# Performance work log

Measured on AMD Instinct MI355X. Metric: run time of the kernel, lower is better.

The kernel has to match this reference:

```python
import jax, jax.numpy as jnp
import numpy as np

B, N, C_SA, OUT = 16, 2048, 512, 1024
BN_EPS = 1e-5


def pconv(x, w, b=None):
    # 1x1 Conv1d: x [B,Cin,N], w [Cout,Cin] -> [B,Cout,N]
    y = jnp.einsum('oc,bcn->bon', w, x)
    return y if b is None else y + b[None, :, None]


def setup_inputs() -> dict:
    key = jax.random.key(0)
    ks = jax.random.split(key, 16)
    s = lambda k, shape: jax.random.normal(k, shape, dtype=jnp.float32) * 0.05
    return {
        'x': jax.random.normal(ks[0], (B, 3, N), dtype=jnp.float32),
        'w1': s(ks[1], (128, 21)), 'b1': s(ks[2], (128,)),
        'w2': s(ks[3], (256, 128)), 'b2': s(ks[4], (256,)),
        'w3': s(ks[5], (512, 512)), 'b3': s(ks[6], (512,)),
        'w4': s(ks[7], (OUT, 512)), 'b4': s(ks[8], (OUT,)),
        'wqk': s(ks[9], (C_SA // 4, C_SA)),            # q_conv.weight tied to k_conv.weight, no bias
        'wv': s(ks[10], (C_SA, C_SA)), 'bv': s(ks[11], (C_SA,)),
        'wt': s(ks[12], (C_SA, C_SA)), 'bt': s(ks[13], (C_SA,)),
        'gamma': jnp.ones((C_SA,), dtype=jnp.float32),
        'beta': jnp.zeros((C_SA,), dtype=jnp.float32),
    }


def reference(x, w1, b1, w2, b2, w3, b3, w4, b4, wqk, wv, bv, wt, bt, gamma, beta):
    b, _, n = x.shape
    # positional encoding on [B,N,3]: [t, sin(t*2^i), cos(t*2^i)] for i in 0..2 -> 21 channels
    t = jnp.transpose(x, (0, 2, 1))
    enc = [t]
    for f in (1.0, 2.0, 4.0):
        enc.append(jnp.sin(t * f))
        enc.append(jnp.cos(t * f))
    h = jnp.transpose(jnp.concatenate(enc, axis=-1), (0, 2, 1))  # [B,21,N]

    h = jax.nn.relu(pconv(h, w1, b1))               # [B,128,N]
    h = pconv(h, w2, b2)                            # [B,256,N]
    g = jnp.max(h, axis=2)                          # [B,256]
    h = jnp.concatenate([h, jnp.broadcast_to(g[:, :, None], (b, g.shape[1], n))], axis=1)  # [B,512,N]
    h = jax.nn.relu(pconv(h, w3, b3))               # [B,512,N]

    # SA_Layer (offset attention, double normalization)
    xq = jnp.einsum('oc,bcn->bno', wqk, h)          # [B,N,128]
    xk = jnp.einsum('oc,bcn->bon', wqk, h)          # [B,128,N]
    xv = pconv(h, wv, bv)                           # [B,512,N]
    energy = jnp.einsum('bqo,bok->bqk', xq, xk)     # [B,N,N]
    attn = jax.nn.softmax(energy, axis=-1)
    attn = attn / (1e-9 + jnp.sum(attn, axis=1, keepdims=True))  # L1 renorm over query dim
    x_r = jnp.einsum('bck,bqk->bcq', xv, attn)      # x_v @ attn^T -> [B,512,N]
    d = pconv(h - x_r, wt, bt)
    # BatchNorm1d, training mode (batch statistics, biased variance)
    mu = jnp.mean(d, axis=(0, 2))
    var = jnp.var(d, axis=(0, 2))
    d = gamma[None, :, None] * (d - mu[None, :, None]) * jax.lax.rsqrt(var + BN_EPS)[None, :, None] + beta[None, :, None]
    h = h + jax.nn.relu(d)

    h = pconv(h, w4, b4)                            # [B,OUT,N]
    return jnp.max(h, axis=2)                       # [B,OUT]
```

## Files before the change

kernel.cpp:

```cpp
#include <hip/hip_runtime.h>
#include <cmath>

#define GN 2048
#define GB 16

typedef __attribute__((ext_vector_type(8))) short bf8_t;
typedef __attribute__((ext_vector_type(4))) float f4_t;

__device__ __forceinline__ short f2bf(float f) {
    union { float f; unsigned u; } v; v.f = f;
    unsigned r = v.u + 0x7FFFu + ((v.u >> 16) & 1u);
    return (short)(r >> 16);
}
__device__ __forceinline__ float bf2f(short s) {
    union { unsigned u; float f; } v; v.u = ((unsigned)(unsigned short)s) << 16;
    return v.f;
}

__device__ __forceinline__ void load16_lds(const short* g, short* l) {
    __builtin_amdgcn_global_load_lds(
        (const __attribute__((address_space(1))) unsigned int*)g,
        (__attribute__((address_space(3))) unsigned int*)l, 16, 0, 0);
}

__device__ __forceinline__ float wave_max(float v) {
#pragma unroll
    for (int o = 32; o > 0; o >>= 1) v = fmaxf(v, __shfl_xor(v, o, 64));
    return v;
}
__device__ __forceinline__ float wave_sum(float v) {
#pragma unroll
    for (int o = 32; o > 0; o >>= 1) v += __shfl_xor(v, o, 64);
    return v;
}
__device__ __forceinline__ float block_sum(float v) {
    __shared__ float sm[4];
    v = wave_sum(v);
    if ((threadIdx.x & 63) == 0) sm[threadIdx.x >> 6] = v;
    __syncthreads();
    v = sm[0] + sm[1] + sm[2] + sm[3];
    __syncthreads();
    return v;
}

__global__ __launch_bounds__(256) void f2ball_k(
    const float* __restrict__ w2, const float* __restrict__ w3,
    const float* __restrict__ wqk, const float* __restrict__ wv,
    const float* __restrict__ wt, const float* __restrict__ w4,
    short* __restrict__ dst) {
    int i = blockIdx.x * 256 + threadIdx.x;
    if (i >= 1409024) return;
    float v;
    if (i < 32768) v = w2[i];
    else if (i < 294912) v = w3[i - 32768];
    else if (i < 360448) v = wqk[i - 294912];
    else if (i < 622592) v = wv[i - 360448];
    else if (i < 884736) v = wt[i - 622592];
    else v = w4[i - 884736];
    dst[i] = f2bf(v);
}

__global__ __launch_bounds__(256) void posenc_conv1_k(
    const float* __restrict__ x, const float* __restrict__ w1,
    const float* __restrict__ b1, short* __restrict__ h1) {
    __shared__ float w[128 * 21];
    __shared__ float bb[128];
    __shared__ float se[256][21];
    const int tid = threadIdx.x;
    for (int i = tid; i < 128 * 21; i += 256) w[i] = w1[i];
    if (tid < 128) bb[tid] = b1[tid];
    int p0 = blockIdx.x * 256;
    int p = p0 + tid, b = p >> 11, n = p & (GN - 1);
    const float* xb = x + (long)b * 3 * GN + n;
    float t0 = xb[0], t1 = xb[GN], t2 = xb[2 * GN];
    se[tid][0] = t0; se[tid][1] = t1; se[tid][2] = t2;
    se[tid][3] = sinf(t0); se[tid][4] = sinf(t1); se[tid][5] = sinf(t2);
    se[tid][6] = cosf(t0); se[tid][7] = cosf(t1); se[tid][8] = cosf(t2);
    se[tid][9] = sinf(2.f * t0); se[tid][10] = sinf(2.f * t1); se[tid][11] = sinf(2.f * t2);
    se[tid][12] = cosf(2.f * t0); se[tid][13] = cosf(2.f * t1); se[tid][14] = cosf(2.f * t2);
    se[tid][15] = sinf(4.f * t0); se[tid][16] = sinf(4.f * t1); se[tid][17] = sinf(4.f * t2);
    se[tid][18] = cosf(4.f * t0); se[tid][19] = cosf(4.f * t1); se[tid][20] = cosf(4.f * t2);
    __syncthreads();
    short* outb = h1 + (long)p0 * 128;
    for (int it = 0; it < 128; ++it) {
        int L = it * 256 + tid;
        int pl = L >> 7, o = L & 127;
        float s = bb[o];
        const float* er = se[pl];
        const float* wr = &w[o * 21];
#pragma unroll
        for (int c = 0; c < 21; ++c) s = fmaf(wr[c], er[c], s);
        outb[L] = f2bf(fmaxf(s, 0.f));
    }
}

template <int MODE, int BIAS, bool RELU, bool STATS = false, bool COLMAX = false>
__global__ __launch_bounds__(256) void mm_k(
    const short* __restrict__ A, int lda, long long aB,
    const short* __restrict__ B, int ldb, long long bB,
    const float* __restrict__ bias, int biasStride,
    const short* __restrict__ aux, long long auxB,
    const float* __restrict__ rsv,
    float* __restrict__ Cf, long long cfB,
    short* __restrict__ Cb, long long cbB,
    float* __restrict__ Pmax, float* __restrict__ Ps2,
    int ldc, int K) {
    const int z = blockIdx.z;
    A += (long long)z * aB;
    B += (long long)z * bB;
    if (MODE == 4) { aux += (long long)z * auxB; rsv += (long long)z * GN; }
    if (MODE == 1) Cf += (long long)z * cfB;
    if (MODE == 2 || MODE == 4 || MODE == 6) Cb += (long long)z * cbB;
    if (MODE == 6) Pmax += (long long)z * GN * 32;
    const int row0 = blockIdx.x * 128, col0 = blockIdx.y * 128;
    const int tid = threadIdx.x;
    const int lane = tid & 63, w = tid >> 6;
    const int r = lane & 15, q = lane >> 4;
    const int wr = w >> 1, wc = w & 1;

    __shared__ short lA[8192];
    __shared__ short lB[8192];

    f4_t acc[4][4] = {};

    const int sRow = lane >> 2;
    const int sKb = (lane & 3) ^ ((lane >> 3) & 3);
    const long aG = (long)(row0 + w * 32 + sRow) * lda + sKb * 8;
    const long bG = (long)(col0 + w * 32 + sRow) * ldb + sKb * 8;
    short* ldsA0 = lA + (w * 32) * 32;
    short* ldsA1 = lA + (w * 32 + 16) * 32;
    short* ldsB0 = lB + (w * 32) * 32;
    short* ldsB1 = lB + (w * 32 + 16) * 32;

    const int sw = (q ^ ((r >> 1) & 3)) * 8;
    int aoff[4], boff[4];
#pragma unroll
    for (int i = 0; i < 4; ++i) {
        aoff[i] = (wr * 64 + i * 16 + r) * 32 + sw;
        boff[i] = (wc * 64 + i * 16 + r) * 32 + sw;
    }

    for (int k0 = 0; k0 < K; k0 += 64) {
        __syncthreads();
        load16_lds(A + aG + k0, ldsA0);
        load16_lds(A + aG + (long)16 * lda + k0, ldsA1);
        load16_lds(B + bG + k0, ldsB0);
        load16_lds(B + bG + (long)16 * ldb + k0, ldsB1);
        load16_lds(A + aG + k0 + 32, ldsA0 + 4096);
        load16_lds(A + aG + (long)16 * lda + k0 + 32, ldsA1 + 4096);
        load16_lds(B + bG + k0 + 32, ldsB0 + 4096);
        load16_lds(B + bG + (long)16 * ldb + k0 + 32, ldsB1 + 4096);
        asm volatile("s_waitcnt vmcnt(0)" ::: "memory");
        __syncthreads();
#pragma unroll
        for (int h = 0; h < 2; ++h) {
            const short* la = lA + h * 4096;
            const short* lb = lB + h * 4096;
            bf8_t av[4], bv[4];
#pragma unroll
            for (int i = 0; i < 4; ++i) av[i] = *(const bf8_t*)(la + aoff[i]);
#pragma unroll
            for (int j = 0; j < 4; ++j) bv[j] = *(const bf8_t*)(lb + boff[j]);
#pragma unroll
            for (int i = 0; i < 4; ++i)
#pragma unroll
                for (int j = 0; j < 4; ++j)
                    acc[i][j] = __builtin_amdgcn_mfma_f32_16x16x32_bf16(av[i], bv[j], acc[i][j], 0, 0, 0);
        }
    }

    if constexpr (MODE == 5) {
        int b = row0 >> 11;
        int rw = (blockIdx.x * 2 + wr) & 31;
#pragma unroll
        for (int j = 0; j < 4; ++j) {
            float vm = -1e30f;
#pragma unroll
            for (int i = 0; i < 4; ++i)
#pragma unroll
                for (int e = 0; e < 4; ++e) vm = fmaxf(vm, acc[i][j][e]);
            vm = fmaxf(vm, __shfl_xor(vm, 16, 64));
            vm = fmaxf(vm, __shfl_xor(vm, 32, 64));
            if (q == 0) {
                int gcol = col0 + wc * 64 + j * 16 + r;
                Pmax[(((long)b * 1024 + gcol) << 5) + rw] = vm + bias[gcol];
            }
        }
    } else if constexpr (MODE == 6) {
        float rsum[4][4] = {};
#pragma unroll
        for (int j = 0; j < 4; ++j) {
            int gcol = col0 + wc * 64 + j * 16 + r;
#pragma unroll
            for (int i = 0; i < 4; ++i) {
#pragma unroll
                for (int e = 0; e < 4; ++e) {
                    int grow = row0 + wr * 64 + i * 16 + q * 4 + e;
                    float ex = __expf(acc[i][j][e]);
                    rsum[i][e] += ex;
                    Cb[(long)grow * ldc + gcol] = f2bf(ex);
                }
            }
        }
#pragma unroll
        for (int i = 0; i < 4; ++i)
#pragma unroll
            for (int e = 0; e < 4; ++e) {
                float v = rsum[i][e];
                v += __shfl_xor(v, 1, 64);
                v += __shfl_xor(v, 2, 64);
                v += __shfl_xor(v, 4, 64);
                v += __shfl_xor(v, 8, 64);
                if (r == 0) {
                    int grow = row0 + wr * 64 + i * 16 + q * 4 + e;
                    Pmax[((long)grow << 5) + blockIdx.y * 2 + wc] = v;
                }
            }
    } else if constexpr (MODE == 4) {
#pragma unroll
        for (int i = 0; i < 4; ++i) {
#pragma unroll
            for (int e = 0; e < 4; ++e) {
                int grow = row0 + wr * 64 + i * 16 + q * 4 + e;
                float rsr = rsv[grow];
                long ob = (long)grow * ldc + col0 + wc * 64 + r;
#pragma unroll
                for (int j = 0; j < 4; ++j) {
                    long off = ob + j * 16;
                    Cb[off] = f2bf(bf2f(aux[off]) - acc[i][j][e] * rsr);
                }
            }
        }
    } else {
        const int b2d = (BIAS == 3) ? (row0 >> 11) : 0;
#pragma unroll
        for (int j = 0; j < 4; ++j) {
            int gcol = col0 + wc * 64 + j * 16 + r;
            float bvv = 0.f;
            if constexpr (BIAS == 1) bvv = bias[gcol];
            if constexpr (BIAS == 3) bvv = bias[b2d * biasStride + gcol];
            float s1 = 0.f, s2 = 0.f;
            float cmx = -1e30f;
#pragma unroll
            for (int i = 0; i < 4; ++i) {
#pragma unroll
                for (int e = 0; e < 4; ++e) {
                    int grow = row0 + wr * 64 + i * 16 + q * 4 + e;
                    float v = acc[i][j][e] + bvv;
                    if constexpr (BIAS == 2) v += bias[grow];
                    if constexpr (RELU) v = fmaxf(v, 0.f);
                    if constexpr (STATS) { s1 += v; s2 = fmaf(v, v, s2); }
                    if constexpr (COLMAX) cmx = fmaxf(cmx, v);
                    long off = (long)grow * ldc + gcol;
                    if constexpr (MODE == 1) Cf[off] = v;
                    if constexpr (MODE == 2) Cb[off] = f2bf(v);
                }
            }
            if constexpr (STATS) {
                s1 += __shfl_xor(s1, 16, 64); s1 += __shfl_xor(s1, 32, 64);
                s2 += __shfl_xor(s2, 16, 64); s2 += __shfl_xor(s2, 32, 64);
                if (q == 0) {
                    int rw2 = blockIdx.x * 2 + wr;
                    Pmax[rw2 * 512 + gcol] = s1;
                    Ps2[rw2 * 512 + gcol] = s2;
                }
            }
            if constexpr (COLMAX) {
                cmx = fmaxf(cmx, __shfl_xor(cmx, 16, 64));
                cmx = fmaxf(cmx, __shfl_xor(cmx, 32, 64));
                if (q == 0) {
                    int b = row0 >> 11;
                    int rw = (blockIdx.x * 2 + wr) & 31;
                    Pmax[(((long)b * ldc + gcol) << 5) + rw] = cmx;
                }
            }
        }
    }
}

__global__ __launch_bounds__(256) void rs_k(const float* __restrict__ rp,
                                            float* __restrict__ rs) {
    int i = blockIdx.x * 256 + threadIdx.x;
    const float* p = rp + ((long)i << 5);
    float s = 0.f;
#pragma unroll
    for (int j = 0; j < 32; ++j) s += p[j];
    rs[i] = 1.f / s;
}

__global__ __launch_bounds__(256) void maxg_k(const float* __restrict__ P,
                                              float* __restrict__ g) {
    int i = blockIdx.x * 256 + threadIdx.x;
    const float* p = P + ((long)i << 5);
    float m = p[0];
#pragma unroll
    for (int j = 1; j < 32; ++j) m = fmaxf(m, p[j]);
    g[i] = m;
}

__global__ __launch_bounds__(256) void cvec_k(const float* __restrict__ w3,
                                              const float* __restrict__ b3,
                                              const float* __restrict__ g,
                                              float* __restrict__ cvec) {
    int idx = blockIdx.x * 256 + threadIdx.x;
    int b = idx >> 9, o = idx & 511;
    const float* gb = g + (b << 8);
    const float* wr = w3 + (long)o * 512 + 256;
    float s = b3[o];
    for (int c = 0; c < 256; ++c) s = fmaf(wr[c], gb[c], s);
    cvec[idx] = s;
}

__global__ __launch_bounds__(256) void colsum1_k(const short* __restrict__ Ab,
                                                 const float* __restrict__ rs,
                                                 float* __restrict__ cp) {
    int kb = blockIdx.x, qs = blockIdx.y, z = blockIdx.z;
    int k = kb * 256 + threadIdx.x;
    const short* p = Ab + (long)z * GN * GN + (long)qs * 64 * GN + k;
    const float* rv = rs + z * GN + qs * 64;
    float s = 0.f;
    for (int qq = 0; qq < 64; ++qq) s += bf2f(p[(long)qq * GN]) * rv[qq];
    cp[((z * 32 + qs) * GN) + k] = s;
}
__global__ __launch_bounds__(256) void colsum2_k(const float* __restrict__ cp,
                                                 float* __restrict__ cs) {
    int k = blockIdx.x * 256 + threadIdx.x, z = blockIdx.y;
    float s = 1e-9f;
    for (int qs = 0; qs < 32; ++qs) s += cp[((z * 32 + qs) * GN) + k];
    cs[z * GN + k] = s;
}

__global__ __launch_bounds__(256) void xvscale_k(short* __restrict__ xvc,
                                                 const float* __restrict__ cs) {
    long idx = ((long)blockIdx.x * 256 + threadIdx.x) * 4;
    int p = (int)(idx & 32767);
    short* ptr = xvc + idx;
    float4 cv = *(const float4*)(cs + p);
    uint2 u = *(const uint2*)ptr;
    short* sp = (short*)&u;
    sp[0] = f2bf(bf2f(sp[0]) / cv.x);
    sp[1] = f2bf(bf2f(sp[1]) / cv.y);
    sp[2] = f2bf(bf2f(sp[2]) / cv.z);
    sp[3] = f2bf(bf2f(sp[3]) / cv.w);
    *(uint2*)ptr = u;
}

__global__ __launch_bounds__(256) void bn2_k(const float* __restrict__ bs1,
                                             const float* __restrict__ bs2,
                                             const float* __restrict__ gamma,
                                             const float* __restrict__ beta,
                                             float* __restrict__ sc,
                                             float* __restrict__ sh) {
    int c = blockIdx.x;
    float s = 0.f, s2 = 0.f;
    for (int i = threadIdx.x; i < 512; i += 256) {
        s += bs1[i * 512 + c];
        s2 += bs2[i * 512 + c];
    }
    s = block_sum(s);
    s2 = block_sum(s2);
    if (threadIdx.x == 0) {
        const float cnt = (float)(GB * GN);
        float mu = s / cnt;
        float var = s2 / cnt - mu * mu;
        float r = rsqrtf(var + 1e-5f);
        float gm = gamma[c] * r;
        sc[c] = gm;
        sh[c] = beta[c] - gm * mu;
    }
}

__global__ __launch_bounds__(256) void bn_apply_k(const short* __restrict__ h3b,
                                                  const short* __restrict__ d,
                                                  const float* __restrict__ sc,
                                                  const float* __restrict__ sh,
                                                  short* __restrict__ h4) {
    long bidx = ((long)blockIdx.x * 256 + threadIdx.x) * 4;
    int c = (int)(bidx & 511);
    uint2 du = *(const uint2*)(d + bidx);
    short* ds = (short*)&du;
    uint2 hu = *(const uint2*)(h3b + bidx);
    short* hs = (short*)&hu;
    float4 a4 = *(const float4*)(sc + c);
    float4 b4 = *(const float4*)(sh + c);
    float r0 = bf2f(hs[0]) + fmaxf(fmaf(bf2f(ds[0]), a4.x, b4.x), 0.f);
    float r1 = bf2f(hs[1]) + fmaxf(fmaf(bf2f(ds[1]), a4.y, b4.y), 0.f);
    float r2 = bf2f(hs[2]) + fmaxf(fmaf(bf2f(ds[2]), a4.z, b4.z), 0.f);
    float r3 = bf2f(hs[3]) + fmaxf(fmaf(bf2f(ds[3]), a4.w, b4.w), 0.f);
    uint2 o;
    o.x = (unsigned short)f2bf(r0) | ((unsigned)(unsigned short)f2bf(r1) << 16);
    o.y = (unsigned short)f2bf(r2) | ((unsigned)(unsigned short)f2bf(r3) << 16);
    *(uint2*)(h4 + bidx) = o;
}

__global__ __launch_bounds__(256) void max_final_k(const float* __restrict__ P,
                                                   float* __restrict__ out) {
    int i = blockIdx.x * 256 + threadIdx.x;
    const float* p = P + ((long)i << 5);
    float m = p[0];
#pragma unroll
    for (int j = 1; j < 32; ++j) m = fmaxf(m, p[j]);
    out[i] = m;
}

extern "C" void kernel_launch(void* const* d_in, const int* in_sizes, int n_in,
                              void* d_out, int out_size, void* d_ws, size_t ws_size,
                              hipStream_t stream) {
    const float* x = (const float*)d_in[0];
    const float* w1 = (const float*)d_in[1];
    const float* b1 = (const float*)d_in[2];
    const float* w2 = (const float*)d_in[3];
    const float* b2 = (const float*)d_in[4];
    const float* w3 = (const float*)d_in[5];
    const float* b3 = (const float*)d_in[6];
    const float* w4 = (const float*)d_in[7];
    const float* b4 = (const float*)d_in[8];
    const float* wqk = (const float*)d_in[9];
    const float* wv = (const float*)d_in[10];
    const float* bv = (const float*)d_in[11];
    const float* wt = (const float*)d_in[12];
    const float* bt = (const float*)d_in[13];
    const float* gamma = (const float*)d_in[14];
    const float* beta = (const float*)d_in[15];
    float* out = (float*)d_out;

    char* base = (char*)d_ws;
    short* h3b = (short*)base;
    short* hsT = (short*)(base + 33554432);
    short* kT  = (short*)(base + 67108864);
    short* xvc = (short*)(base + 75497472);
    short* EA  = (short*)(base + 109051904);
    short* h1T = (short*)(base + 109051904);
    short* h2T = (short*)(base + 117440512);
    short* dTb = (short*)(base + 109051904);
    short* h4T = (short*)(base + 67108864);
    char* S = base + 243269632;
    float* g    = (float*)(S + 262144);
    float* cvec = (float*)(S + 278528);
    float* cp   = (float*)(S + 311296);
    float* rp   = cp;
    float* cs   = (float*)(S + 4505600);
    float* bs1  = (float*)(S + 4636672);
    float* bs2  = (float*)(S + 5685248);
    float* bnsc = (float*)(S + 6733824);
    float* bnsh = (float*)(S + 6735872);
    float* Pmax = (float*)(S + 6737920);
    short* w2b  = (short*)(S + 8835072);
    short* w3b  = (short*)(S + 8900608);
    short* wqkb = (short*)(S + 9424896);
    short* wvb  = (short*)(S + 9555968);
    short* wtb  = (short*)(S + 10080256);
    short* w4b  = (short*)(S + 10604544);
    float* rs   = (float*)(S + 11653120);

    f2ball_k<<<5505, 256, 0, stream>>>(w2, w3, wqk, wv, wt, w4, w2b);

    posenc_conv1_k<<<128, 256, 0, stream>>>(x, w1, b1, h1T);

    mm_k<2, 1, false, false, true><<<dim3(256, 2, 1), 256, 0, stream>>>(
        h1T, 128, 0, w2b, 128, 0, b2, 0, nullptr, 0, nullptr,
        nullptr, 0, h2T, 0, Pmax, nullptr, 256, 128);

    maxg_k<<<16, 256, 0, stream>>>(Pmax, g);

    cvec_k<<<32, 256, 0, stream>>>(w3, b3, g, cvec);

    mm_k<2, 3, true><<<dim3(256, 4, 1), 256, 0, stream>>>(
        h2T, 256, 0, w3b, 512, 0, cvec, 512, nullptr, 0, nullptr,
        nullptr, 0, h3b, 0, nullptr, nullptr, 512, 256);

    mm_k<2, 0, false><<<dim3(256, 1, 1), 256, 0, stream>>>(
        h3b, 512, 0, wqkb, 512, 0, nullptr, 0, nullptr, 0, nullptr,
        nullptr, 0, kT, 0, nullptr, nullptr, 128, 512);

    mm_k<2, 2, false><<<dim3(4, 256, 1), 256, 0, stream>>>(
        wvb, 512, 0, h3b, 512, 0, bv, 0, nullptr, 0, nullptr,
        nullptr, 0, xvc, 0, nullptr, nullptr, 32768, 512);

    mm_k<6, 0, false><<<dim3(16, 16, 16), 256, 0, stream>>>(
        kT, 128, (long long)GN * 128, kT, 128, (long long)GN * 128,
        nullptr, 0, nullptr, 0, nullptr, nullptr, 0,
        EA, (long long)GN * GN, rp, nullptr, GN, 128);
    rs_k<<<128, 256, 0, stream>>>(rp, rs);
    colsum1_k<<<dim3(8, 32, GB), 256, 0, stream>>>(EA, rs, cp);
    colsum2_k<<<dim3(8, GB), 256, 0, stream>>>(cp, cs);
    xvscale_k<<<16384, 256, 0, stream>>>(xvc, cs);
    mm_k<4, 0, false><<<dim3(16, 4, 16), 256, 0, stream>>>(
        EA, GN, (long long)GN * GN,
        xvc, 32768, (long long)GN,
        nullptr, 0,
        h3b, (long long)GN * 512, rs,
        nullptr, 0,
        hsT, (long long)GN * 512,
        nullptr, nullptr, 512, GN);

    mm_k<2, 1, false, true><<<dim3(256, 4, 1), 256, 0, stream>>>(
        hsT, 512, 0, wtb, 512, 0, bt, 0, nullptr, 0, nullptr,
        nullptr, 0, dTb, 0, bs1, bs2, 512, 512);

    bn2_k<<<512, 256, 0, stream>>>(bs1, bs2, gamma, beta, bnsc, bnsh);

    bn_apply_k<<<16384, 256, 0, stream>>>(h3b, dTb, bnsc, bnsh, h4T);

    mm_k<5, 1, false><<<dim3(256, 8, 1), 256, 0, stream>>>(
        h4T, 512, 0, w4b, 512, 0, b4, 0, nullptr, 0, nullptr,
        nullptr, 0, nullptr, 0, Pmax, nullptr, 1024, 512);

    max_final_k<<<64, 256, 0, stream>>>(Pmax, out);
}
```

Measured before the change: 500.2 us.

## Add 256x256-tile 8-wave GEMM kernel for attention-apply, wt and w4 matmuls

Adds a new GEMM kernel with a 256x256 output tile, 512 threads and double-buffered LDS staging. The global-to-LDS loads are interleaved with four MFMA quadrants per K-step, using barriers, priority raising and explicit waitcnt. It replaces the older kernel for the attention-times-V matmul, the wt projection with BN statistics, and the w4 projection with max pooling, to raise data reuse per tile and overlap loads with compute. The cost is heavier register and LDS use (128 KB of LDS per block) and fewer blocks per grid.

```diff
diff --git a/kernel.cpp b/kernel.cpp
--- a/kernel.cpp
+++ b/kernel.cpp
@@ -278,6 +278,213 @@
     }
 }
 
+__device__ __forceinline__ void stage2(const short* g0, const short* g1, short* dst) {
+    load16_lds(g0, dst);
+    load16_lds(g1, dst + 4096);
+}
+
+template <int MH, int NH>
+__device__ __forceinline__ void mfma_quad(const bf8_t (&av)[4][2], const bf8_t (&bv)[2][2],
+                                          f4_t (&acc)[8][4]) {
+#pragma unroll
+    for (int mi = 0; mi < 4; ++mi)
+#pragma unroll
+        for (int ni = 0; ni < 2; ++ni) {
+            acc[MH * 4 + mi][NH * 2 + ni] = __builtin_amdgcn_mfma_f32_16x16x32_bf16(
+                av[mi][0], bv[ni][0], acc[MH * 4 + mi][NH * 2 + ni], 0, 0, 0);
+            acc[MH * 4 + mi][NH * 2 + ni] = __builtin_amdgcn_mfma_f32_16x16x32_bf16(
+                av[mi][1], bv[ni][1], acc[MH * 4 + mi][NH * 2 + ni], 0, 0, 0);
+        }
+}
+
+__device__ __forceinline__ void rd4(const short* p, int swz0, int swz1, bf8_t (&v)[4][2]) {
+#pragma unroll
+    for (int i = 0; i < 4; ++i) {
+        v[i][0] = *(const bf8_t*)(p + i * 1024 + swz0);
+        v[i][1] = *(const bf8_t*)(p + i * 1024 + swz1);
+    }
+}
+__device__ __forceinline__ void rd2(const short* p, int swz0, int swz1, bf8_t (&v)[2][2]) {
+#pragma unroll
+    for (int i = 0; i < 2; ++i) {
+        v[i][0] = *(const bf8_t*)(p + i * 1024 + swz0);
+        v[i][1] = *(const bf8_t*)(p + i * 1024 + swz1);
+    }
+}
+
+#define SB0 __builtin_amdgcn_sched_barrier(0)
+#define BARRIER asm volatile("s_barrier" ::: "memory")
+
+template <int MODE, int BIAS, bool RELU, bool STATS = false>
+__global__ __launch_bounds__(512, 2) void mm256_k(
+    const short* __restrict__ A, int lda, long long aB,
+    const short* __restrict__ B, int ldb, long long bB,
+    const float* __restrict__ bias,
+    const short* __restrict__ aux, long long auxB,
+    const float* __restrict__ rsv,
+    short* __restrict__ Cb, long long cbB,
+    float* __restrict__ Pmax, float* __restrict__ Ps2,
+    int ldc, int K) {
+    __shared__ short lA[32768];
+    __shared__ short lB[32768];
+    const int z = blockIdx.z;
+    A += (long long)z * aB;
+    B += (long long)z * bB;
+    if constexpr (MODE == 4) { aux += (long long)z * auxB; rsv += (long long)z * GN; }
+    if constexpr (MODE != 5) Cb += (long long)z * cbB;
+    const int row0 = blockIdx.x * 256, col0 = blockIdx.y * 256;
+    const int tid = threadIdx.x;
+    const int lane = tid & 63, w = tid >> 6;
+    const int r16 = lane & 15, q = lane >> 4;
+    const int wr = w >> 2, wc = w & 3;
+
+    const int rc0 = w * 8 + (lane >> 3);
+    const int s8 = ((lane & 7) ^ (rc0 & 7)) * 8;
+    const long ldA64 = (long)64 * lda, ldB64 = (long)64 * ldb;
+    const short* aH0 = A + (long)(row0 + rc0) * lda + s8;
+    const short* aH1 = aH0 + (long)128 * lda;
+    const short* bH0 = B + (long)(col0 + rc0) * ldb + s8;
+    const short* bH1 = bH0 + (long)128 * ldb;
+    short* dA = lA + w * 512;
+    short* dB = lB + w * 512;
+
+#define STG_A(d_, h_, kt_) stage2((h_ ? aH1 : aH0) + (long)(kt_) * 64,                      \
+                                  (h_ ? aH1 : aH0) + (long)(kt_) * 64 + ldA64,              \
+                                  dA + (d_) * 16384 + (h_) * 8192)
+#define STG_B(d_, h_, kt_) stage2((h_ ? bH1 : bH0) + (long)(kt_) * 64,                      \
+                                  (h_ ? bH1 : bH0) + (long)(kt_) * 64 + ldB64,              \
+                                  dB + (d_) * 16384 + (h_) * 8192)
+
+    const int swz0 = (q ^ (r16 & 7)) * 8;
+    const int swz1 = ((4 + q) ^ (r16 & 7)) * 8;
+    const int arow = (wr * 64 + r16) * 64;
+    const int brow = (wc * 32 + r16) * 64;
+
+    f4_t acc[8][4] = {};
+    bf8_t av[4][2], bv0[2][2], bv1[2][2];
+    const int NT = K >> 6;
+
+    STG_A(0, 0, 0); STG_B(0, 0, 0); STG_B(0, 1, 0); STG_A(0, 1, 0);
+    STG_A(1, 0, 1); STG_B(1, 0, 1);
+    asm volatile("s_waitcnt vmcnt(4)" ::: "memory");
+    SB0; BARRIER; SB0;
+
+    for (int t = 0; t < NT; ++t) {
+        const int d = t & 1;
+        const short* la = lA + d * 16384;
+        const short* lb = lB + d * 16384;
+        rd4(la + arow, swz0, swz1, av);
+        rd2(lb + brow, swz0, swz1, bv0);
+        if (t + 1 < NT) STG_B(d ^ 1, 1, t + 1);
+        SB0; BARRIER; SB0;
+        __builtin_amdgcn_s_setprio(1);
+        mfma_quad<0, 0>(av, bv0, acc);
+        __builtin_amdgcn_s_setprio(0);
+        SB0; BARRIER; SB0;
+        rd2(lb + 8192 + brow, swz0, swz1, bv1);
+        if (t + 1 < NT) STG_A(d ^ 1, 1, t + 1);
+        SB0; BARRIER; SB0;
+        __builtin_amdgcn_s_setprio(1);
+        mfma_quad<0, 1>(av, bv1, acc);
+        __builtin_amdgcn_s_setprio(0);
+        SB0; BARRIER; SB0;
+        rd4(la + 8192 + arow, swz0, swz1, av);
+        if (t + 2 < NT) STG_A(d, 0, t + 2);
+        SB0; BARRIER; SB0;
+        __builtin_amdgcn_s_setprio(1);
+        mfma_quad<1, 0>(av, bv0, acc);
+        __builtin_amdgcn_s_setprio(0);
+        SB0; BARRIER; SB0;
+        if (t + 2 < NT) {
+            STG_B(d, 0, t + 2);
+            asm volatile("s_waitcnt vmcnt(4)" ::: "memory");
+        } else if (t + 1 < NT) {
+            asm volatile("s_waitcnt vmcnt(0)" ::: "memory");
+        }
+        SB0; BARRIER; SB0;
+        __builtin_amdgcn_s_setprio(1);
+        mfma_quad<1, 1>(av, bv1, acc);
+        __builtin_amdgcn_s_setprio(0);
+        SB0; BARRIER; SB0;
+    }
+#undef STG_A
+#undef STG_B
+
+    const int mrow = row0 + wr * 64 + q * 4;
+    const int ncol = col0 + wc * 32 + r16;
+
+    if constexpr (MODE == 4) {
+#pragma unroll
+        for (int m = 0; m < 8; ++m) {
+#pragma unroll
+            for (int e = 0; e < 4; ++e) {
+                const int grow = mrow + (m >> 2) * 128 + (m & 3) * 16 + e;
+                const float rsr = rsv[grow];
+                const long rb = (long)grow * ldc;
+#pragma unroll
+                for (int n = 0; n < 4; ++n) {
+                    const long off = rb + ncol + (n >> 1) * 128 + (n & 1) * 16;
+                    Cb[off] = f2bf(bf2f(aux[off]) - acc[m][n][e] * rsr);
+                }
+            }
+        }
+    } else if constexpr (MODE == 2) {
+#pragma unroll
+        for (int n = 0; n < 4; ++n) {
+            const int gcol = ncol + (n >> 1) * 128 + (n & 1) * 16;
+            float bvv = 0.f;
+            if constexpr (BIAS == 1) bvv = bias[gcol];
+#pragma unroll
+            for (int mh = 0; mh < 2; ++mh) {
+                float s1 = 0.f, s2 = 0.f;
+#pragma unroll
+                for (int mi = 0; mi < 4; ++mi) {
+#pragma unroll
+                    for (int e = 0; e < 4; ++e) {
+                        const int grow = mrow + mh * 128 + mi * 16 + e;
+                        float v = acc[mh * 4 + mi][n][e] + bvv;
+                        if constexpr (RELU) v = fmaxf(v, 0.f);
+                        if constexpr (STATS) { s1 += v; s2 = fmaf(v, v, s2); }
+                        Cb[(long)grow * ldc + gcol] = f2bf(v);
+                    }
+                }
+                if constexpr (STATS) {
+                    s1 += __shfl_xor(s1, 16, 64); s1 += __shfl_xor(s1, 32, 64);
+                    s2 += __shfl_xor(s2, 16, 64); s2 += __shfl_xor(s2, 32, 64);
+                    if (q == 0) {
+                        const int rw2 = blockIdx.x * 4 + mh * 2 + wr;
+                        Pmax[rw2 * 512 + gcol] = s1;
+                        Ps2[rw2 * 512 + gcol] = s2;
+                    }
+                }
+            }
+        }
+    } else if constexpr (MODE == 5) {
+        const int b = row0 >> 11;
+#pragma unroll
+        for (int n = 0; n < 4; ++n) {
+            const int gcol = ncol + (n >> 1) * 128 + (n & 1) * 16;
+            const float bvv = bias[gcol];
+#pragma unroll
+            for (int mh = 0; mh < 2; ++mh) {
+                float vm = -1e30f;
+#pragma unroll
+                for (int mi = 0; mi < 4; ++mi)
+#pragma unroll
+                    for (int e = 0; e < 4; ++e) vm = fmaxf(vm, acc[mh * 4 + mi][n][e]);
+                vm = fmaxf(vm, __shfl_xor(vm, 16, 64));
+                vm = fmaxf(vm, __shfl_xor(vm, 32, 64));
+                if (q == 0) {
+                    const int rw = (blockIdx.x * 4 + mh * 2 + wr) & 31;
+                    Pmax[(((long)b * ldc + gcol) << 5) + rw] = vm + bvv;
+                }
+            }
+        }
+    }
+}
+#undef SB0
+#undef BARRIER
+
 __global__ __launch_bounds__(256) void rs_k(const float* __restrict__ rp,
                                             float* __restrict__ rs) {
     int i = blockIdx.x * 256 + threadIdx.x;
@@ -485,26 +692,23 @@
     colsum1_k<<<dim3(8, 32, GB), 256, 0, stream>>>(EA, rs, cp);
     colsum2_k<<<dim3(8, GB), 256, 0, stream>>>(cp, cs);
     xvscale_k<<<16384, 256, 0, stream>>>(xvc, cs);
-    mm_k<4, 0, false><<<dim3(16, 4, 16), 256, 0, stream>>>(
+    mm256_k<4, 0, false><<<dim3(8, 2, 16), 512, 0, stream>>>(
         EA, GN, (long long)GN * GN,
         xvc, 32768, (long long)GN,
-        nullptr, 0,
-        h3b, (long long)GN * 512, rs,
-        nullptr, 0,
-        hsT, (long long)GN * 512,
-        nullptr, nullptr, 512, GN);
-
-    mm_k<2, 1, false, true><<<dim3(256, 4, 1), 256, 0, stream>>>(
-        hsT, 512, 0, wtb, 512, 0, bt, 0, nullptr, 0, nullptr,
-        nullptr, 0, dTb, 0, bs1, bs2, 512, 512);
+        nullptr, h3b, (long long)GN * 512, rs,
+        hsT, (long long)GN * 512, nullptr, nullptr, 512, GN);
+
+    mm256_k<2, 1, false, true><<<dim3(128, 2, 1), 512, 0, stream>>>(
+        hsT, 512, 0, wtb, 512, 0, bt, nullptr, 0, nullptr,
+        dTb, 0, bs1, bs2, 512, 512);
 
     bn2_k<<<512, 256, 0, stream>>>(bs1, bs2, gamma, beta, bnsc, bnsh);
 
     bn_apply_k<<<16384, 256, 0, stream>>>(h3b, dTb, bnsc, bnsh, h4T);
 
-    mm_k<5, 1, false><<<dim3(256, 8, 1), 256, 0, stream>>>(
-        h4T, 512, 0, w4b, 512, 0, b4, 0, nullptr, 0, nullptr,
-        nullptr, 0, nullptr, 0, Pmax, nullptr, 1024, 512);
+    mm256_k<5, 1, false><<<dim3(128, 4, 1), 512, 0, stream>>>(
+        h4T, 512, 0, w4b, 512, 0, b4, nullptr, 0, nullptr,
+        nullptr, 0, Pmax, nullptr, 1024, 512);
 
     max_final_k<<<64, 256, 0, stream>>>(Pmax, out);
 }
```

Result: faster. 467.7 us (-6.5%).
